# Performance work log

Hardware: AMD Instinct MI355X
Metric: run time of the kernel (lower is better)

The kernel has to match this reference:

```python
import jax, jax.numpy as jnp
import numpy as np

# Sizes (match init_kwargs config)
B, S, D = 4, 2048, 1024          # batch, seq_len, d_hidden
DE, E, K = 256, 8, 2             # d_expert, n_routed_experts, top_k
N_SHARED = 2
SDE = DE * N_SHARED              # shared expert hidden dim


def silu(v):
    return v * jax.nn.sigmoid(v)


def setup_inputs() -> dict:
    key = jax.random.key(0)
    ks = jax.random.split(key, 9)
    s_d = 1.0 / np.sqrt(D)
    s_de = 1.0 / np.sqrt(DE)
    s_sde = 1.0 / np.sqrt(SDE)
    return {
        "x": jax.random.normal(ks[0], (B, S, D), dtype=jnp.float32),
        "Wg": jax.random.normal(ks[1], (D, E), dtype=jnp.float32) * s_d,          # gate router
        "w_gate": jax.random.normal(ks[2], (E, D, DE), dtype=jnp.float32) * s_d,   # per-expert W_gate
        "w_up": jax.random.normal(ks[3], (E, D, DE), dtype=jnp.float32) * s_d,     # per-expert W_up
        "w_down": jax.random.normal(ks[4], (E, DE, D), dtype=jnp.float32) * s_de,  # per-expert W_down
        "sg": jax.random.normal(ks[5], (D, SDE), dtype=jnp.float32) * s_d,         # shared W_gate
        "su": jax.random.normal(ks[6], (D, SDE), dtype=jnp.float32) * s_d,         # shared W_up
        "sd": jax.random.normal(ks[7], (SDE, D), dtype=jnp.float32) * s_sde,       # shared W_down
        "top_k": K,
    }


def reference(x, Wg, w_gate, w_up, w_down, sg, su, sd, top_k):
    b, s, d = x.shape
    n_exp = Wg.shape[-1]

    # Shared expert (SwiGLU) over all tokens
    shared = (silu(x @ sg) * (x @ su)) @ sd  # [B,S,D]

    # Gating: softmax then top-k (unsorted order irrelevant for weighted sum)
    scores = jax.nn.softmax(x @ Wg, axis=-1)            # [B,S,E]
    topk_scores, topk_ids = jax.lax.top_k(scores, top_k)  # [B,S,K]

    t = b * s
    xf = x.reshape(t, d)
    ts = topk_scores.reshape(t, top_k)
    ti = topk_ids.reshape(t, top_k)

    # Dense combine weights [T,E]: weight of expert e for token t (0 if not routed)
    combine = jnp.zeros((t, n_exp), dtype=x.dtype).at[
        jnp.arange(t)[:, None], ti
    ].add(ts)

    # Per-expert SwiGLU computed densely, combined with routing weights
    g = jnp.einsum('td,edh->teh', xf, w_gate)  # [T,E,DE]
    u = jnp.einsum('td,edh->teh', xf, w_up)    # [T,E,DE]
    h = silu(g) * u
    routed = jnp.einsum('teh,ehd,te->td', h, w_down, combine)  # [T,D]

    return routed.reshape(b, s, d) + shared
```

## Files before the change

kernel.cpp:

```cpp
#include <hip/hip_runtime.h>
#include <stdint.h>

#define TOK   8192
#define DIM   1024
#define NEXP  8
#define TOPK  2
#define WPAD  1028

typedef unsigned short ushort_t;
typedef __attribute__((ext_vector_type(8))) short bf16x8;
typedef __attribute__((ext_vector_type(4))) float f32x4;

__device__ __forceinline__ unsigned short f2bf(float f) {
  unsigned int u = __float_as_uint(f);
  u += 0x7fffu + ((u >> 16) & 1u);
  return (unsigned short)(u >> 16);
}
__device__ __forceinline__ float bf2f(ushort_t u) {
  return __uint_as_float(((unsigned int)u) << 16);
}

__device__ __forceinline__ void gload_lds16(const void* g, void* l) {
  __builtin_amdgcn_global_load_lds(
      (const __attribute__((address_space(1))) void*)(uintptr_t)g,
      (__attribute__((address_space(3))) void*)(unsigned int)(uintptr_t)l,
      16, 0, 0);
}

__global__ __launch_bounds__(256) void k_prep(
    const float* __restrict__ x, const float* __restrict__ Wg,
    ushort_t* __restrict__ xb, int* __restrict__ tid, float* __restrict__ tw,
    const float* __restrict__ sg, const float* __restrict__ su,
    const float* __restrict__ sd, const float* __restrict__ wgm,
    const float* __restrict__ wu, const float* __restrict__ wdn,
    ushort_t* __restrict__ Wsh1, ushort_t* __restrict__ Wsd,
    ushort_t* __restrict__ Wgu, ushort_t* __restrict__ Wd) {
  __shared__ float sm[2 * 64 * 65];
  if (blockIdx.x < 512) {
    for (int j = threadIdx.x; j < DIM * NEXP; j += 256)
      sm[(j & 7) * WPAD + (j >> 3)] = Wg[j];
    __syncthreads();
    const int wid = threadIdx.x >> 6, lane = threadIdx.x & 63;
#pragma unroll
    for (int tt2 = 0; tt2 < 4; ++tt2) {
      const int t = blockIdx.x * 16 + wid * 4 + tt2;
      const float* xr = x + (size_t)t * DIM;
      ushort_t* xw = xb + (size_t)t * DIM;
      float acc[NEXP];
#pragma unroll
      for (int e = 0; e < NEXP; ++e) acc[e] = 0.f;
#pragma unroll
      for (int k = 0; k < 4; ++k) {
        const int i = k * 256 + lane * 4;
        const float4 xv = *(const float4*)(xr + i);
        union { ushort_t u[4]; uint2 v; } s;
        s.u[0] = f2bf(xv.x); s.u[1] = f2bf(xv.y);
        s.u[2] = f2bf(xv.z); s.u[3] = f2bf(xv.w);
        *(uint2*)(xw + i) = s.v;
#pragma unroll
        for (int e = 0; e < NEXP; ++e) {
          const float4 wv = *(const float4*)&sm[e * WPAD + i];
          acc[e] += xv.x * wv.x + xv.y * wv.y + xv.z * wv.z + xv.w * wv.w;
        }
      }
#pragma unroll
      for (int e = 0; e < NEXP; ++e) {
        float v = acc[e];
#pragma unroll
        for (int o = 32; o > 0; o >>= 1) v += __shfl_xor(v, o);
        acc[e] = v;
      }
      if (lane == 0) {
        float mx = acc[0];
#pragma unroll
        for (int e = 1; e < NEXP; ++e) mx = fmaxf(mx, acc[e]);
        float p[NEXP]; float s = 0.f;
#pragma unroll
        for (int e = 0; e < NEXP; ++e) { p[e] = __expf(acc[e] - mx); s += p[e]; }
        const float inv = 1.f / s;
#pragma unroll
        for (int e = 0; e < NEXP; ++e) p[e] *= inv;
        int i1 = 0; float s1 = p[0];
#pragma unroll
        for (int e = 1; e < NEXP; ++e) if (p[e] > s1) { s1 = p[e]; i1 = e; }
        int i2 = -1; float s2 = -1.f;
#pragma unroll
        for (int e = 0; e < NEXP; ++e) if (e != i1 && p[e] > s2) { s2 = p[e]; i2 = e; }
        tid[t * 2] = i1; tid[t * 2 + 1] = i2;
        tw[t * 2] = s1;  tw[t * 2 + 1] = s2;
      }
    }
    return;
  }
  int b = blockIdx.x - 512;
  const float *s0, *s1; ushort_t* dst; int R, C; bool ilv;
  int r0, c0;
  if (b < 128) {
    ilv = true; s0 = sg; s1 = su; dst = Wsh1; R = 1024; C = 512;
    c0 = (b & 7) * 64; r0 = (b >> 3) * 64;
  } else if (b < 640) {
    b -= 128; const int e = b >> 6; b &= 63;
    ilv = true;
    s0 = wgm + (size_t)e * 1024 * 256; s1 = wu + (size_t)e * 1024 * 256;
    dst = Wgu + (size_t)e * 512 * 1024; R = 1024; C = 256;
    c0 = (b & 3) * 64; r0 = (b >> 2) * 64;
  } else if (b < 704) {
    b -= 640; ilv = false; s0 = sd; s1 = sd; dst = Wsd; R = 512; C = 1024;
    c0 = (b & 7) * 128; r0 = (b >> 3) * 64;
  } else {
    b -= 704; const int e = b >> 5; b &= 31;
    ilv = false;
    s0 = wdn + (size_t)e * 256 * 1024; s1 = s0;
    dst = Wd + (size_t)e * 1024 * 256; R = 256; C = 1024;
    c0 = (b & 7) * 128; r0 = (b >> 3) * 64;
  }
  const int row16 = threadIdx.x >> 4;
  const int q16   = threadIdx.x & 15;
#pragma unroll
  for (int p = 0; p < 2; ++p) {
    const float* s = p ? s1 : s0;
    const int cc = ilv ? c0 : (c0 + p * 64);
    float (*tt)[65] = (float(*)[65])(sm + p * 64 * 65);
#pragma unroll
    for (int i = 0; i < 64; i += 16) {
      const float4 v = *(const float4*)&s[(size_t)(r0 + row16 + i) * C + cc + q16 * 4];
      tt[q16 * 4 + 0][row16 + i] = v.x;
      tt[q16 * 4 + 1][row16 + i] = v.y;
      tt[q16 * 4 + 2][row16 + i] = v.z;
      tt[q16 * 4 + 3][row16 + i] = v.w;
    }
  }
  __syncthreads();
#pragma unroll
  for (int p = 0; p < 2; ++p) {
    const int cc = ilv ? c0 : (c0 + p * 64);
    float (*tt)[65] = (float(*)[65])(sm + p * 64 * 65);
#pragma unroll
    for (int i = 0; i < 64; i += 16) {
      const int n = cc + row16 + i;
      const int drow = ilv ? (2 * n + p) : n;
      const float4 v = *(const float4*)&tt[row16 + i][q16 * 4];
      union { ushort_t u[4]; uint2 w; } s4;
      s4.u[0] = f2bf(v.x); s4.u[1] = f2bf(v.y);
      s4.u[2] = f2bf(v.z); s4.u[3] = f2bf(v.w);
      *(uint2*)&dst[(size_t)drow * R + r0 + q16 * 4] = s4.w;
    }
  }
}

__global__ __launch_bounds__(1024) void k_scan(const int* __restrict__ tid,
                                               int* __restrict__ cnt,
                                               int* __restrict__ off,
                                               int* __restrict__ cnt2) {
  __shared__ int h[NEXP];
  if (threadIdx.x < NEXP) h[threadIdx.x] = 0;
  __syncthreads();
  int loc[NEXP];
#pragma unroll
  for (int e = 0; e < NEXP; ++e) loc[e] = 0;
  const int4* t4 = (const int4*)tid;
#pragma unroll
  for (int k = 0; k < TOK * TOPK / 4 / 1024; ++k) {
    const int4 v = t4[threadIdx.x + k * 1024];
#pragma unroll
    for (int e = 0; e < NEXP; ++e)
      loc[e] += (v.x == e) + (v.y == e) + (v.z == e) + (v.w == e);
  }
#pragma unroll
  for (int e = 0; e < NEXP; ++e) if (loc[e]) atomicAdd(&h[e], loc[e]);
  __syncthreads();
  if (threadIdx.x == 0) {
    int run = 0;
    for (int e = 0; e < NEXP; ++e) { off[e] = run; cnt[e] = h[e]; run += h[e]; }
  }
  if (threadIdx.x < NEXP) cnt2[threadIdx.x] = 0;
}

__global__ __launch_bounds__(256) void k_scatter(const int* __restrict__ tid,
                                                 const float* __restrict__ tw,
                                                 const int* __restrict__ off,
                                                 int* __restrict__ cnt2,
                                                 int* __restrict__ tok,
                                                 float* __restrict__ wgt,
                                                 int* __restrict__ dstrow) {
  const int t = blockIdx.x * 256 + threadIdx.x;
  const int lane = threadIdx.x & 63;
#pragma unroll
  for (int j = 0; j < TOPK; ++j) {
    const int e = tid[t * 2 + j];
    const float w = tw[t * 2 + j];
    int slot = 0;
#pragma unroll
    for (int ee = 0; ee < NEXP; ++ee) {
      const unsigned long long m = __ballot(e == ee);
      if (m) {
        const int r = __popcll(m & ((1ull << lane) - 1ull));
        const int leader = __ffsll((unsigned long long)m) - 1;
        int base = 0;
        if (lane == leader) base = atomicAdd(&cnt2[ee], (int)__popcll(m));
        base = __shfl(base, leader);
        if (e == ee) slot = off[ee] + base + r;
      }
    }
    tok[slot] = t;
    wgt[slot] = w;
    dstrow[slot] = t * 2 + j;
  }
}

__global__ __launch_bounds__(256) void k_gemm1(
    const ushort_t* __restrict__ A0, const ushort_t* __restrict__ Bgu,
    const ushort_t* __restrict__ Bsh,
    ushort_t* __restrict__ he, ushort_t* __restrict__ hs,
    const int* __restrict__ tok,
    const int* __restrict__ cnt, const int* __restrict__ off) {
  constexpr int K = 1024, NB = 4, NGROUP = 16, MBSLOT = 16;
  constexpr int NWG = NGROUP * MBSLOT * NB;
  __shared__ __attribute__((aligned(16))) ushort_t lA[2][128 * 64];
  __shared__ __attribute__((aligned(16))) ushort_t lB[2][128 * 64];

  const int wg = (blockIdx.x % 8) * (NWG / 8) + blockIdx.x / 8;
  const int g = wg / (MBSLOT * NB);
  const int rem = wg % (MBSLOT * NB);
  const int mbslot = rem / NB;
  const int nb = rem % NB;
  const int nBase = nb * 128;

  int m_e, offE = 0, rowq = 0, hh = 0;
  bool gat = false;
  const ushort_t* Abase = A0;
  const ushort_t* Bblk;
  if (g < 8) {
    gat = true; m_e = cnt[g]; offE = off[g];
    Bblk = Bgu + (size_t)g * 512 * 1024;
  } else {
    const int q = (g - 8) >> 1; hh = (g - 8) & 1;
    rowq = q * 2048; m_e = 2048;
    Abase = A0 + (size_t)rowq * 1024;
    Bblk = Bsh + (size_t)hh * 512 * 1024;
  }
  if (m_e == 0) return;

  const int wid = threadIdx.x >> 6, lane = threadIdx.x & 63;
  const int wm = wid >> 1, wn = wid & 1;
  const int l15 = lane & 15, lq = lane >> 4;

  const ushort_t* bptr[4];
#pragma unroll
  for (int cc = 0; cc < 4; ++cc) {
    const int c = wid * 4 + cc;
    const int rl = c * 8 + (lane >> 3);
    const int slot = (lane & 7) ^ (rl & 7);
    bptr[cc] = Bblk + (size_t)(nBase + rl) * K + slot * 8;
  }

  for (int mb = mbslot; mb * 128 < m_e; mb += MBSLOT) {
    const int mBase = mb * 128;
    const ushort_t* aptr[4];
#pragma unroll
    for (int cc = 0; cc < 4; ++cc) {
      const int c = wid * 4 + cc;
      const int rl = c * 8 + (lane >> 3);
      const int slot = (lane & 7) ^ (rl & 7);
      const int gr = mBase + rl;
      const int gc = (gr < m_e) ? gr : (m_e - 1);
      const ushort_t* ar;
      if (gat) ar = A0 + (size_t)tok[offE + gc] * 1024;
      else     ar = Abase + (size_t)gc * K;
      aptr[cc] = ar + slot * 8;
    }

    auto stage = [&](int buf, int ktv) {
#pragma unroll
      for (int cc = 0; cc < 4; ++cc) {
        const int c = wid * 4 + cc;
        gload_lds16(aptr[cc] + ktv, &lA[buf][c * 512]);
        gload_lds16(bptr[cc] + ktv, &lB[buf][c * 512]);
      }
    };

    f32x4 acc[4][4];
#pragma unroll
    for (int mi = 0; mi < 4; ++mi)
#pragma unroll
      for (int ni = 0; ni < 4; ++ni) acc[mi][ni] = (f32x4){0.f, 0.f, 0.f, 0.f};

    stage(0, 0);
    int cur = 0;
    for (int kt = 0; kt < K; kt += 64) {
      if (kt + 64 < K) {
        stage(cur ^ 1, kt + 64);
        asm volatile("s_waitcnt vmcnt(8)" ::: "memory");
      } else {
        asm volatile("s_waitcnt vmcnt(0)" ::: "memory");
      }
      __builtin_amdgcn_s_barrier();
#pragma unroll
      for (int kk = 0; kk < 2; ++kk) {
        bf16x8 af[4], bfr[4];
#pragma unroll
        for (int mi = 0; mi < 4; ++mi) {
          const int row = wm * 64 + mi * 16 + l15;
          const int cb = ((kk * 32 + lq * 8) * 2) ^ ((row & 7) << 4);
          af[mi] = *(const bf16x8*)((const char*)lA + cur * 16384 + row * 128 + cb);
        }
#pragma unroll
        for (int ni = 0; ni < 4; ++ni) {
          const int row = wn * 64 + ni * 16 + l15;
          const int cb = ((kk * 32 + lq * 8) * 2) ^ ((row & 7) << 4);
          bfr[ni] = *(const bf16x8*)((const char*)lB + cur * 16384 + row * 128 + cb);
        }
#pragma unroll
        for (int mi = 0; mi < 4; ++mi)
#pragma unroll
          for (int ni = 0; ni < 4; ++ni)
            acc[mi][ni] = __builtin_amdgcn_mfma_f32_16x16x32_bf16(
                af[mi], bfr[ni], acc[mi][ni], 0, 0, 0);
      }
      __builtin_amdgcn_s_barrier();
      cur ^= 1;
    }

#pragma unroll
    for (int mi = 0; mi < 4; ++mi) {
#pragma unroll
      for (int r = 0; r < 4; ++r) {
        const int gg = mBase + wm * 64 + mi * 16 + lq * 4 + r;
        const bool ok = gg < m_e;
#pragma unroll
        for (int ni = 0; ni < 4; ++ni) {
          const float v = acc[mi][ni][r];
          const int c = nBase + wn * 64 + ni * 16 + l15;
          const float o = __shfl_xor(v, 1);
          if (!(c & 1) && ok) {
            const float hv = (v / (1.f + __expf(-v))) * o;
            if (gat) he[(size_t)(offE + gg) * 256 + (c >> 1)] = f2bf(hv);
            else     hs[(size_t)(rowq + gg) * 512 + hh * 256 + (c >> 1)] = f2bf(hv);
          }
        }
      }
    }
  }
}

__global__ __launch_bounds__(512, 1) void k_gemm2r(
    const ushort_t* __restrict__ he, const ushort_t* __restrict__ Wd,
    ushort_t* __restrict__ contrib, const float* __restrict__ wgt,
    const int* __restrict__ cnt, const int* __restrict__ off,
    const int* __restrict__ dstrow) {
  constexpr int K = 256;
  __shared__ __attribute__((aligned(16))) ushort_t lB[128 * 256];
  __shared__ __attribute__((aligned(16))) ushort_t lA[8][2][32 * 64];

  const int e = blockIdx.x & 7;
  const int c0 = blockIdx.x >> 3;
  const int nb = c0 & 7;
  const int mslot = c0 >> 3;
  const int nBase = nb * 128;

  const int m_e = cnt[e];
  const int offE = (m_e > 0) ? off[e] : 0;
  const ushort_t* Abase = he + (size_t)offE * K;
  const ushort_t* Bblk = Wd + (size_t)e * 1024 * K;

  const int wid = threadIdx.x >> 6, lane = threadIdx.x & 63;
  const int l15 = lane & 15, lq = lane >> 4;

  if (m_e > 0) {
#pragma unroll
    for (int i = 0; i < 8; ++i) {
      const int L = (wid * 8 + i) * 64 + lane;
      const int row = L >> 5, s = L & 31;
      const int ss = s ^ (row & 31);
      gload_lds16(Bblk + (size_t)(nBase + row) * K + ss * 8,
                  ((char*)lB) + (size_t)(wid * 8 + i) * 1024);
    }
  }

  char* lAw = (char*)&lA[wid][0][0];
  auto stageA = [&](int buf, int chunk, int kc) {
#pragma unroll
    for (int i = 0; i < 4; ++i) {
      const int L = i * 64 + lane;
      const int row = L >> 3, s = L & 7;
      const int ss = s ^ (row & 7);
      int gr = chunk * 32 + row;
      if (gr >= m_e) gr = m_e - 1;
      gload_lds16(Abase + (size_t)gr * K + kc * 64 + ss * 8,
                  lAw + (size_t)buf * 4096 + (size_t)i * 1024);
    }
  };

  int cw = mslot * 8 + wid;
  bool active = (m_e > 0) && (cw * 32 < m_e);
  if (m_e > 0) stageA(0, active ? cw : 0, 0);
  asm volatile("s_waitcnt vmcnt(4)" ::: "memory");
  __builtin_amdgcn_s_barrier();
  if (!active) return;

  int buf = 0;
  while (active) {
    f32x4 acc[2][8];
#pragma unroll
    for (int mi = 0; mi < 2; ++mi)
#pragma unroll
      for (int ni = 0; ni < 8; ++ni) acc[mi][ni] = (f32x4){0.f, 0.f, 0.f, 0.f};

    for (int kc = 0; kc < 4; ++kc) {
      int nc = cw, nk = kc + 1;
      if (nk == 4) { nk = 0; nc = cw + 32; }
      if (nc * 32 < m_e) {
        stageA(buf ^ 1, nc, nk);
        asm volatile("s_waitcnt vmcnt(4)" ::: "memory");
      } else {
        asm volatile("s_waitcnt vmcnt(0)" ::: "memory");
      }
      const char* sA = lAw + buf * 4096;
#pragma unroll
      for (int kk = 0; kk < 2; ++kk) {
        bf16x8 af[2], bfr[8];
#pragma unroll
        for (int mi = 0; mi < 2; ++mi) {
          const int row = mi * 16 + l15;
          af[mi] = *(const bf16x8*)(sA + row * 128 + (((kk * 4 + lq) ^ (row & 7)) << 4));
        }
#pragma unroll
        for (int ni = 0; ni < 8; ++ni) {
          const int brow = ni * 16 + l15;
          const int ck = kc * 8 + kk * 4 + lq;
          bfr[ni] = *(const bf16x8*)((const char*)lB + brow * 512 +
                                     ((ck ^ (brow & 31)) << 4));
        }
#pragma unroll
        for (int mi = 0; mi < 2; ++mi)
#pragma unroll
          for (int ni = 0; ni < 8; ++ni)
            acc[mi][ni] = __builtin_amdgcn_mfma_f32_16x16x32_bf16(
                af[mi], bfr[ni], acc[mi][ni], 0, 0, 0);
      }
      buf ^= 1;
    }

#pragma unroll
    for (int mi = 0; mi < 2; ++mi) {
#pragma unroll
      for (int r = 0; r < 4; ++r) {
        const int gg = cw * 32 + mi * 16 + lq * 4 + r;
        if (gg < m_e) {
          const float w = wgt[offE + gg];
          const int dr = dstrow[offE + gg];
#pragma unroll
          for (int ni = 0; ni < 8; ++ni) {
            const int c = nBase + ni * 16 + l15;
            contrib[(size_t)dr * 1024 + c] = f2bf(acc[mi][ni][r] * w);
          }
        }
      }
    }
    cw += 32;
    active = cw * 32 < m_e;
  }
  asm volatile("s_waitcnt vmcnt(0)" ::: "memory");
}

__global__ __launch_bounds__(512, 1) void k_gemm2s(
    const ushort_t* __restrict__ hs, const ushort_t* __restrict__ Wsd,
    const ushort_t* __restrict__ contrib, float* __restrict__ out) {
  constexpr int K = 512;
  __shared__ __attribute__((aligned(16))) ushort_t lB[64 * 512];
  __shared__ __attribute__((aligned(16))) ushort_t lA[8][2][32 * 64];

  const int wg = (blockIdx.x & 7) * 32 + (blockIdx.x >> 3);
  const int nstrip = wg >> 4;
  const int mslot = wg & 15;
  const int nBase = nstrip * 64;

  const int wid = threadIdx.x >> 6, lane = threadIdx.x & 63;
  const int l15 = lane & 15, lq = lane >> 4;

#pragma unroll
  for (int i = 0; i < 8; ++i) {
    const int L = (wid * 8 + i) * 64 + lane;
    const int row = L >> 6, s = L & 63;
    const int ss = s ^ row;
    gload_lds16(Wsd + (size_t)(nBase + row) * K + ss * 8,
                ((char*)lB) + (size_t)(wid * 8 + i) * 1024);
  }

  char* lAw = (char*)&lA[wid][0][0];
  auto stageA = [&](int buf, int chunk, int kc) {
#pragma unroll
    for (int i = 0; i < 4; ++i) {
      const int L = i * 64 + lane;
      const int row = L >> 3, s = L & 7;
      const int ss = s ^ (row & 7);
      gload_lds16(hs + (size_t)(chunk * 32 + row) * K + kc * 64 + ss * 8,
                  lAw + (size_t)buf * 4096 + (size_t)i * 1024);
    }
  };

  int cw = mslot * 8 + wid;
  stageA(0, cw, 0);
  asm volatile("s_waitcnt vmcnt(4)" ::: "memory");
  __builtin_amdgcn_s_barrier();

  int buf = 0;
  for (int rep = 0; rep < 2; ++rep) {
    f32x4 acc[2][4];
#pragma unroll
    for (int mi = 0; mi < 2; ++mi)
#pragma unroll
      for (int ni = 0; ni < 4; ++ni) acc[mi][ni] = (f32x4){0.f, 0.f, 0.f, 0.f};

    for (int kc = 0; kc < 8; ++kc) {
      int nc = cw, nk = kc + 1;
      if (nk == 8) { nk = 0; nc = cw + 128; }
      if (nc < 256) {
        stageA(buf ^ 1, nc, nk);
        asm volatile("s_waitcnt vmcnt(4)" ::: "memory");
      } else {
        asm volatile("s_waitcnt vmcnt(0)" ::: "memory");
      }
      const char* sA = lAw + buf * 4096;
#pragma unroll
      for (int kk = 0; kk < 2; ++kk) {
        bf16x8 af[2], bfr[4];
#pragma unroll
        for (int mi = 0; mi < 2; ++mi) {
          const int row = mi * 16 + l15;
          af[mi] = *(const bf16x8*)(sA + row * 128 + (((kk * 4 + lq) ^ (row & 7)) << 4));
        }
#pragma unroll
        for (int ni = 0; ni < 4; ++ni) {
          const int brow = ni * 16 + l15;
          const int ck = kc * 8 + kk * 4 + lq;
          bfr[ni] = *(const bf16x8*)((const char*)lB + brow * 1024 +
                                     ((ck ^ brow) << 4));
        }
#pragma unroll
        for (int mi = 0; mi < 2; ++mi)
#pragma unroll
          for (int ni = 0; ni < 4; ++ni)
            acc[mi][ni] = __builtin_amdgcn_mfma_f32_16x16x32_bf16(
                af[mi], bfr[ni], acc[mi][ni], 0, 0, 0);
      }
      buf ^= 1;
    }

#pragma unroll
    for (int mi = 0; mi < 2; ++mi) {
#pragma unroll
      for (int r = 0; r < 4; ++r) {
        const int gg = cw * 32 + mi * 16 + lq * 4 + r;
#pragma unroll
        for (int ni = 0; ni < 4; ++ni) {
          const int c = nBase + ni * 16 + l15;
          out[(size_t)gg * 1024 + c] = acc[mi][ni][r]
              + bf2f(contrib[(size_t)(gg * 2) * 1024 + c])
              + bf2f(contrib[(size_t)(gg * 2 + 1) * 1024 + c]);
        }
      }
    }
    cw += 128;
  }
  asm volatile("s_waitcnt vmcnt(0)" ::: "memory");
}

extern "C" void kernel_launch(void* const* d_in, const int* in_sizes, int n_in,
                              void* d_out, int out_size, void* d_ws, size_t ws_size,
                              hipStream_t stream) {
  (void)in_sizes; (void)n_in; (void)out_size; (void)ws_size;
  const float* x      = (const float*)d_in[0];
  const float* Wg     = (const float*)d_in[1];
  const float* w_gate = (const float*)d_in[2];
  const float* w_up   = (const float*)d_in[3];
  const float* w_down = (const float*)d_in[4];
  const float* sg     = (const float*)d_in[5];
  const float* su     = (const float*)d_in[6];
  const float* sd     = (const float*)d_in[7];
  float* out = (float*)d_out;

  char* ws = (char*)d_ws;
  size_t o = 0;
  ushort_t* xb    = (ushort_t*)(ws + o); o += (size_t)TOK * DIM * 2;
  ushort_t* Wsh1  = (ushort_t*)(ws + o); o += (size_t)1024 * 1024 * 2;
  ushort_t* Wsd   = (ushort_t*)(ws + o); o += (size_t)1024 * 512 * 2;
  ushort_t* Wgu   = (ushort_t*)(ws + o); o += (size_t)NEXP * 512 * 1024 * 2;
  ushort_t* Wd    = (ushort_t*)(ws + o); o += (size_t)NEXP * 1024 * 256 * 2;
  ushort_t* hs    = (ushort_t*)(ws + o); o += (size_t)TOK * 512 * 2;
  ushort_t* he    = (ushort_t*)(ws + o); o += (size_t)TOK * TOPK * 256 * 2;
  int*   tid   = (int*)(ws + o);   o += (size_t)TOK * TOPK * 4;
  float* tw    = (float*)(ws + o); o += (size_t)TOK * TOPK * 4;
  int*   tok   = (int*)(ws + o);   o += (size_t)TOK * TOPK * 4;
  float* wgt   = (float*)(ws + o); o += (size_t)TOK * TOPK * 4;
  int*   dstrow= (int*)(ws + o);   o += (size_t)TOK * TOPK * 4;
  int*   cnt   = (int*)(ws + o);   o += 64;
  int*   offp  = (int*)(ws + o);   o += 64;
  int*   cnt2  = (int*)(ws + o);   o += 64;
  ushort_t* contrib = (ushort_t*)(ws + o);

  k_prep<<<1472, 256, 0, stream>>>(x, Wg, xb, tid, tw, sg, su, sd,
                                   w_gate, w_up, w_down, Wsh1, Wsd, Wgu, Wd);
  k_scan<<<1, 1024, 0, stream>>>(tid, cnt, offp, cnt2);
  k_scatter<<<TOK / 256, 256, 0, stream>>>(tid, tw, offp, cnt2, tok, wgt, dstrow);

  k_gemm1<<<1024, 256, 0, stream>>>(xb, Wgu, Wsh1, he, hs, tok, cnt, offp);
  k_gemm2r<<<256, 512, 0, stream>>>(he, Wd, contrib, wgt, cnt, offp, dstrow);
  k_gemm2s<<<256, 512, 0, stream>>>(hs, Wsd, contrib, out);
}
```

Measured before the change: 171.4 us.

## Switch gemm1 to triple-buffered K=32 LDS pipeline with single barrier

Reworks the first grouped GEMM's main loop from a double-buffered 64-wide K tile to a triple-buffered 32-wide K tile with a prefetch distance of two stages. Each iteration now uses one barrier instead of two. The LDS swizzle changes to match 64-byte rows, and s_setprio raises wave priority around the MFMA block. The goal is to hide global-to-LDS latency better and cut sync overhead per step, at the cost of twice as many loop iterations and less MFMA work between barriers.

```diff
diff --git a/kernel.cpp b/kernel.cpp
--- a/kernel.cpp
+++ b/kernel.cpp
@@ -214,10 +214,10 @@
     ushort_t* __restrict__ he, ushort_t* __restrict__ hs,
     const int* __restrict__ tok,
     const int* __restrict__ cnt, const int* __restrict__ off) {
-  constexpr int K = 1024, NB = 4, NGROUP = 16, MBSLOT = 16;
+  constexpr int K = 1024, NB = 4, NGROUP = 16, MBSLOT = 16, NT = 32;
   constexpr int NWG = NGROUP * MBSLOT * NB;
-  __shared__ __attribute__((aligned(16))) ushort_t lA[2][128 * 64];
-  __shared__ __attribute__((aligned(16))) ushort_t lB[2][128 * 64];
+  __shared__ __attribute__((aligned(16))) ushort_t lA[3][128 * 32];
+  __shared__ __attribute__((aligned(16))) ushort_t lB[3][128 * 32];
 
   const int wg = (blockIdx.x % 8) * (NWG / 8) + blockIdx.x / 8;
   const int g = wg / (MBSLOT * NB);
@@ -245,37 +245,34 @@
   const int wm = wid >> 1, wn = wid & 1;
   const int l15 = lane & 15, lq = lane >> 4;
 
-  const ushort_t* bptr[4];
-#pragma unroll
-  for (int cc = 0; cc < 4; ++cc) {
-    const int c = wid * 4 + cc;
-    const int rl = c * 8 + (lane >> 3);
-    const int slot = (lane & 7) ^ (rl & 7);
-    bptr[cc] = Bblk + (size_t)(nBase + rl) * K + slot * 8;
+  int srow[2], scol[2];
+  const ushort_t* bsrc[2];
+#pragma unroll
+  for (int c = 0; c < 2; ++c) {
+    const int L = c * 256 + threadIdx.x;
+    srow[c] = L >> 2;
+    scol[c] = (L & 3) ^ ((srow[c] >> 1) & 3);
+    bsrc[c] = Bblk + (size_t)(nBase + srow[c]) * K + scol[c] * 8;
   }
 
   for (int mb = mbslot; mb * 128 < m_e; mb += MBSLOT) {
     const int mBase = mb * 128;
-    const ushort_t* aptr[4];
-#pragma unroll
-    for (int cc = 0; cc < 4; ++cc) {
-      const int c = wid * 4 + cc;
-      const int rl = c * 8 + (lane >> 3);
-      const int slot = (lane & 7) ^ (rl & 7);
-      const int gr = mBase + rl;
+    const ushort_t* asrc[2];
+#pragma unroll
+    for (int c = 0; c < 2; ++c) {
+      const int gr = mBase + srow[c];
       const int gc = (gr < m_e) ? gr : (m_e - 1);
-      const ushort_t* ar;
-      if (gat) ar = A0 + (size_t)tok[offE + gc] * 1024;
-      else     ar = Abase + (size_t)gc * K;
-      aptr[cc] = ar + slot * 8;
-    }
-
-    auto stage = [&](int buf, int ktv) {
-#pragma unroll
-      for (int cc = 0; cc < 4; ++cc) {
-        const int c = wid * 4 + cc;
-        gload_lds16(aptr[cc] + ktv, &lA[buf][c * 512]);
-        gload_lds16(bptr[cc] + ktv, &lB[buf][c * 512]);
+      const ushort_t* ar = gat ? (A0 + (size_t)tok[offE + gc] * 1024)
+                               : (Abase + (size_t)gc * K);
+      asrc[c] = ar + scol[c] * 8;
+    }
+
+    auto stage = [&](int buf, int kt) {
+#pragma unroll
+      for (int c = 0; c < 2; ++c) {
+        const int L = c * 256 + threadIdx.x;
+        gload_lds16(asrc[c] + kt, &lA[buf][L * 8]);
+        gload_lds16(bsrc[c] + kt, &lB[buf][L * 8]);
       }
     };
 
@@ -286,40 +283,36 @@
       for (int ni = 0; ni < 4; ++ni) acc[mi][ni] = (f32x4){0.f, 0.f, 0.f, 0.f};
 
     stage(0, 0);
-    int cur = 0;
-    for (int kt = 0; kt < K; kt += 64) {
-      if (kt + 64 < K) {
-        stage(cur ^ 1, kt + 64);
-        asm volatile("s_waitcnt vmcnt(8)" ::: "memory");
-      } else {
-        asm volatile("s_waitcnt vmcnt(0)" ::: "memory");
-      }
+    stage(1, 32);
+    for (int t = 0; t < NT; ++t) {
+      if (t + 1 < NT) asm volatile("s_waitcnt vmcnt(4)" ::: "memory");
+      else            asm volatile("s_waitcnt vmcnt(0)" ::: "memory");
       __builtin_amdgcn_s_barrier();
-#pragma unroll
-      for (int kk = 0; kk < 2; ++kk) {
-        bf16x8 af[4], bfr[4];
-#pragma unroll
-        for (int mi = 0; mi < 4; ++mi) {
-          const int row = wm * 64 + mi * 16 + l15;
-          const int cb = ((kk * 32 + lq * 8) * 2) ^ ((row & 7) << 4);
-          af[mi] = *(const bf16x8*)((const char*)lA + cur * 16384 + row * 128 + cb);
-        }
-#pragma unroll
-        for (int ni = 0; ni < 4; ++ni) {
-          const int row = wn * 64 + ni * 16 + l15;
-          const int cb = ((kk * 32 + lq * 8) * 2) ^ ((row & 7) << 4);
-          bfr[ni] = *(const bf16x8*)((const char*)lB + cur * 16384 + row * 128 + cb);
-        }
-#pragma unroll
-        for (int mi = 0; mi < 4; ++mi)
-#pragma unroll
-          for (int ni = 0; ni < 4; ++ni)
-            acc[mi][ni] = __builtin_amdgcn_mfma_f32_16x16x32_bf16(
-                af[mi], bfr[ni], acc[mi][ni], 0, 0, 0);
-      }
-      __builtin_amdgcn_s_barrier();
-      cur ^= 1;
-    }
+      if (t + 2 < NT) stage((t + 2) % 3, (t + 2) * 32);
+
+      const char* sA = (const char*)lA[t % 3];
+      const char* sB = (const char*)lB[t % 3];
+      bf16x8 af[4], bfr[4];
+#pragma unroll
+      for (int mi = 0; mi < 4; ++mi) {
+        const int row = wm * 64 + mi * 16 + l15;
+        af[mi] = *(const bf16x8*)(sA + row * 64 + ((lq ^ ((row >> 1) & 3)) << 4));
+      }
+#pragma unroll
+      for (int ni = 0; ni < 4; ++ni) {
+        const int row = wn * 64 + ni * 16 + l15;
+        bfr[ni] = *(const bf16x8*)(sB + row * 64 + ((lq ^ ((row >> 1) & 3)) << 4));
+      }
+      __builtin_amdgcn_s_setprio(1);
+#pragma unroll
+      for (int mi = 0; mi < 4; ++mi)
+#pragma unroll
+        for (int ni = 0; ni < 4; ++ni)
+          acc[mi][ni] = __builtin_amdgcn_mfma_f32_16x16x32_bf16(
+              af[mi], bfr[ni], acc[mi][ni], 0, 0, 0);
+      __builtin_amdgcn_s_setprio(0);
+    }
+    __builtin_amdgcn_s_barrier();
 
 #pragma unroll
     for (int mi = 0; mi < 4; ++mi) {
```

Measured after the change: 186.6 us. +8.9%, slower.
